# Optimization experiments

Hardware: AMD Instinct MI355X
Metric: run time of the kernel (lower is better)

Reference implementation:

```python
import jax, jax.numpy as jnp
import numpy as np

N_NODES = 100000
N_EDGES = 600000
IN_C, HID_C, OUT_C = 128, 128, 64


def setup_inputs() -> dict:
    key = jax.random.key(0)
    k1, k2, k3, k4 = jax.random.split(key, 4)
    x = jax.random.normal(k1, (N_NODES, IN_C), dtype=jnp.float32)
    edge_index = jax.random.randint(k2, (2, N_EDGES), 0, N_NODES, dtype=jnp.int64)
    # Glorot-ish init for linear weights
    W1 = jax.random.normal(k3, (IN_C, HID_C), dtype=jnp.float32) / np.sqrt(IN_C)
    b1 = jnp.zeros((HID_C,), dtype=jnp.float32)
    W2 = jax.random.normal(k4, (HID_C, OUT_C), dtype=jnp.float32) / np.sqrt(HID_C)
    b2 = jnp.zeros((OUT_C,), dtype=jnp.float32)
    prelu_a = jnp.full((1,), 0.25, dtype=jnp.float32)  # torch nn.PReLU default
    return {"x": x, "edge_index": edge_index, "W1": W1, "b1": b1,
            "W2": W2, "b2": b2, "prelu_a": prelu_a}


def _gcn_conv(x, src, dst, norm, W, b, num_nodes):
    # PyG GCNConv: h = x W; out[i] = sum_{(j->i)} norm_ji * h[j] + b
    h = x @ W                                   # [N, C_out]
    msg = h[src] * norm[:, None]                # [E', C_out] gather + scale
    out = jax.ops.segment_sum(msg, dst, num_segments=num_nodes)
    return out + b


def reference(x, edge_index, W1, b1, W2, b2, prelu_a):
    n = x.shape[0]
    # add self-loops
    loops = jnp.arange(n, dtype=edge_index.dtype)
    src = jnp.concatenate([edge_index[0], loops])
    dst = jnp.concatenate([edge_index[1], loops])
    # symmetric normalization deg^{-1/2}[src] * deg^{-1/2}[dst]
    deg = jax.ops.segment_sum(jnp.ones_like(dst, dtype=x.dtype), dst, num_segments=n)
    dinv = jnp.where(deg > 0, jax.lax.rsqrt(deg), 0.0)
    norm = dinv[src] * dinv[dst]
    # dropout p=0.0 -> identity
    h = _gcn_conv(x, src, dst, norm, W1, b1, n)
    h = jnp.where(h >= 0, h, prelu_a * h)       # PReLU (single shared parameter)
    out = _gcn_conv(h, src, dst, norm, W2, b2, n)
    return out
```

## Files before the change

### kernel.cpp

```cpp
#include <hip/hip_runtime.h>


typedef __attribute__((ext_vector_type(8))) short bf16x8;
typedef __attribute__((ext_vector_type(4))) float f32x4;

#define CAP 96

__device__ inline unsigned short f2bf(float f) {
    unsigned int b = __float_as_uint(f);
    b += 0x7FFFu + ((b >> 16) & 1u);
    return (unsigned short)(b >> 16);
}
__device__ inline float bflo(unsigned int u) { return __uint_as_float(u << 16); }
__device__ inline float bfhi(unsigned int u) { return __uint_as_float(u & 0xFFFF0000u); }

__global__ void k_pre(const float* __restrict__ W1, const float* __restrict__ W2,
                      unsigned short* __restrict__ Wt1, unsigned short* __restrict__ Wt2,
                      int* __restrict__ cnt, int n) {
    int i = blockIdx.x * blockDim.x + threadIdx.x;
    if (i < n) cnt[i] = 0;
    if (i < 128 * 128) {
        int nn = i >> 7, k = i & 127;
        Wt1[i] = f2bf(W1[k * 128 + nn]);
    } else if (i < 128 * 128 + 64 * 128) {
        int j = i - 128 * 128;
        int nn = j >> 7, k = j & 127;
        Wt2[j] = f2bf(W2[k * 64 + nn]);
    }
}

__global__ void k_fill(const int* __restrict__ src, const int* __restrict__ dst,
                       int* __restrict__ cnt, int* __restrict__ bucket, int e) {
    int i = blockIdx.x * blockDim.x + threadIdx.x;
    if (i >= e) return;
    int d = dst[i];
    int pos = atomicAdd(&cnt[d], 1);
    if (pos < CAP) bucket[(size_t)d * CAP + pos] = src[i];
}

template <int BN, bool CVT, bool DINV>
__global__ __launch_bounds__(512) void k_gemm_mfma(
    const void* __restrict__ Asrc, const unsigned short* __restrict__ Wt,
    unsigned short* __restrict__ H, int n,
    const int* __restrict__ cnt, float* __restrict__ dinv) {
    constexpr int PITCH = 136;
    __shared__ unsigned short Bs[BN * PITCH];
    const int tid = threadIdx.x;

    if (DINV) {
        for (int i = blockIdx.x * 512 + tid; i < n; i += gridDim.x * 512)
            dinv[i] = rsqrtf(1.0f + (float)cnt[i]);
    }

    for (int q = tid; q < BN * 16; q += 512) {
        int row = q >> 4, c16 = q & 15;
        *(uint4*)(Bs + row * PITCH + c16 * 8) =
            *(const uint4*)(Wt + row * 128 + c16 * 8);
    }

    const int wave = tid >> 6, lane = tid & 63;
    const int ml = lane & 15;
    const int g = lane >> 4;
    const int stripe = blockIdx.x * 8 + wave;

    int ra = stripe * 16 + ml;
    if (ra >= n) ra = n - 1;

    bf16x8 af[4];
    if (CVT) {
        const float* A = (const float*)Asrc;
#pragma unroll
        for (int ks = 0; ks < 4; ++ks) {
            const float* p = A + (size_t)ra * 128 + ks * 32 + g * 8;
            float4 a0 = *(const float4*)p;
            float4 a1 = *(const float4*)(p + 4);
            uint4 pk;
            pk.x = (unsigned)f2bf(a0.x) | ((unsigned)f2bf(a0.y) << 16);
            pk.y = (unsigned)f2bf(a0.z) | ((unsigned)f2bf(a0.w) << 16);
            pk.z = (unsigned)f2bf(a1.x) | ((unsigned)f2bf(a1.y) << 16);
            pk.w = (unsigned)f2bf(a1.z) | ((unsigned)f2bf(a1.w) << 16);
            af[ks] = *(bf16x8*)&pk;
        }
    } else {
        const unsigned short* A = (const unsigned short*)Asrc;
#pragma unroll
        for (int ks = 0; ks < 4; ++ks)
            af[ks] = *(const bf16x8*)(A + (size_t)ra * 128 + ks * 32 + g * 8);
    }

    __syncthreads();

    constexpr int NCT = BN / 16;
    f32x4 acc[NCT];
#pragma unroll
    for (int ct = 0; ct < NCT; ++ct) acc[ct] = (f32x4){0.f, 0.f, 0.f, 0.f};

#pragma unroll
    for (int ks = 0; ks < 4; ++ks)
#pragma unroll
        for (int ct = 0; ct < NCT; ++ct) {
            bf16x8 b = *(const bf16x8*)(Bs + (size_t)(ct * 16 + ml) * PITCH + ks * 32 + g * 8);
            acc[ct] = __builtin_amdgcn_mfma_f32_16x16x32_bf16(af[ks], b, acc[ct], 0, 0, 0);
        }

#pragma unroll
    for (int ct = 0; ct < NCT; ++ct)
#pragma unroll
        for (int reg = 0; reg < 4; ++reg) {
            int r = stripe * 16 + g * 4 + reg;
            if (r < n) H[(size_t)r * BN + ct * 16 + ml] = f2bf(acc[ct][reg]);
        }
}

template <int COLS, bool PRELU_BF16_OUT>
__global__ void k_gather(const unsigned short* __restrict__ H,
                         const int* __restrict__ cnt, const int* __restrict__ bucket,
                         const float* __restrict__ dinv, const float* __restrict__ b,
                         void* __restrict__ outp, const float* __restrict__ alpha_p,
                         int n) {
    constexpr int NT = COLS / 8;
    constexpr int G = 256 / NT;
    const int tid = threadIdx.x;
    const int node = blockIdx.x * G + tid / NT;
    if (node >= n) return;
    const int c0 = (tid & (NT - 1)) * 8;

    const float di = dinv[node];
    float acc[8];
    {
        uint4 v = *(const uint4*)(H + (size_t)node * COLS + c0);
        float sl = di * di;
        acc[0] = bflo(v.x) * sl + b[c0 + 0];
        acc[1] = bfhi(v.x) * sl + b[c0 + 1];
        acc[2] = bflo(v.y) * sl + b[c0 + 2];
        acc[3] = bfhi(v.y) * sl + b[c0 + 3];
        acc[4] = bflo(v.z) * sl + b[c0 + 4];
        acc[5] = bfhi(v.z) * sl + b[c0 + 5];
        acc[6] = bflo(v.w) * sl + b[c0 + 6];
        acc[7] = bfhi(v.w) * sl + b[c0 + 7];
    }
    int c = cnt[node];
    if (c > CAP) c = CAP;
    const int* bp = bucket + (size_t)node * CAP;
    for (int p = 0; p < c; ++p) {
        int s = bp[p];
        float nrm = dinv[s] * di;
        uint4 v = *(const uint4*)(H + (size_t)s * COLS + c0);
        acc[0] += bflo(v.x) * nrm;
        acc[1] += bfhi(v.x) * nrm;
        acc[2] += bflo(v.y) * nrm;
        acc[3] += bfhi(v.y) * nrm;
        acc[4] += bflo(v.z) * nrm;
        acc[5] += bfhi(v.z) * nrm;
        acc[6] += bflo(v.w) * nrm;
        acc[7] += bfhi(v.w) * nrm;
    }
    if (PRELU_BF16_OUT) {
        float al = alpha_p[0];
        unsigned short o[8];
#pragma unroll
        for (int j = 0; j < 8; ++j) {
            float t = acc[j];
            t = (t >= 0.f) ? t : al * t;
            o[j] = f2bf(t);
        }
        uint4 pk;
        pk.x = (unsigned)o[0] | ((unsigned)o[1] << 16);
        pk.y = (unsigned)o[2] | ((unsigned)o[3] << 16);
        pk.z = (unsigned)o[4] | ((unsigned)o[5] << 16);
        pk.w = (unsigned)o[6] | ((unsigned)o[7] << 16);
        *(uint4*)((unsigned short*)outp + (size_t)node * COLS + c0) = pk;
    } else {
        float* out = (float*)outp;
        *(float4*)(out + (size_t)node * COLS + c0) =
            make_float4(acc[0], acc[1], acc[2], acc[3]);
        *(float4*)(out + (size_t)node * COLS + c0 + 4) =
            make_float4(acc[4], acc[5], acc[6], acc[7]);
    }
}

extern "C" void kernel_launch(void* const* d_in, const int* in_sizes, int n_in,
                              void* d_out, int out_size, void* d_ws, size_t ws_size,
                              hipStream_t stream) {
    const float* x  = (const float*)d_in[0];
    const int*   ei = (const int*)d_in[1];
    const float* W1 = (const float*)d_in[2];
    const float* b1 = (const float*)d_in[3];
    const float* W2 = (const float*)d_in[4];
    const float* b2 = (const float*)d_in[5];
    const float* pa = (const float*)d_in[6];
    float* out = (float*)d_out;

    const int n = in_sizes[0] / 128;
    const int e = in_sizes[1] / 2;
    const int* src = ei;
    const int* dst = ei + e;
    const int B = 256;

    unsigned short* h1  = (unsigned short*)d_ws;
    unsigned short* hp  = h1 + (size_t)n * 128;
    unsigned short* h2  = hp + (size_t)n * 128;
    unsigned short* Wt1 = h2 + (size_t)n * 64;
    unsigned short* Wt2 = Wt1 + 128 * 128;
    float* dinv  = (float*)(Wt2 + 64 * 128);
    int* cnt     = (int*)(dinv + n);
    int* bucket  = cnt + n;

    const int gblk = ((n + 15) / 16 + 7) / 8;

    k_pre<<<(n + B - 1) / B, B, 0, stream>>>(W1, W2, Wt1, Wt2, cnt, n);
    k_fill<<<(e + B - 1) / B, B, 0, stream>>>(src, dst, cnt, bucket, e);
    k_gemm_mfma<128, true, true><<<gblk, 512, 0, stream>>>(x, Wt1, h1, n, cnt, dinv);
    k_gather<128, true><<<(n + 15) / 16, 256, 0, stream>>>(h1, cnt, bucket, dinv,
                                                           b1, hp, pa, n);
    k_gemm_mfma<64, false, false><<<gblk, 512, 0, stream>>>(hp, Wt2, h2, n,
                                                            nullptr, nullptr);
    k_gather<64, false><<<(n + 31) / 32, 256, 0, stream>>>(h2, cnt, bucket, dinv,
                                                           b2, out, nullptr, n);
}
```

Before: 225.3 us.

## Fuse edge bucketing into first GEMM and compute dinv inline in gather

Moves the edge-bucket fill (atomic counting and scatter of source indices) into the tail of the first MFMA GEMM kernel, which removes one launch and lets the scatter overlap with GEMM work. The dinv array is dropped: the gather kernels recompute rsqrt(1+cnt) for the destination and each neighbor. The neighbor loop is unrolled by four, loading indices as int4, to expose more independent memory loads. The trade-off is extra rsqrt work and cnt reads per edge, in both gather passes.

```diff
diff --git a/kernel.cpp b/kernel.cpp
--- a/kernel.cpp
+++ b/kernel.cpp
@@ -29,28 +29,15 @@
     }
 }
 
-__global__ void k_fill(const int* __restrict__ src, const int* __restrict__ dst,
-                       int* __restrict__ cnt, int* __restrict__ bucket, int e) {
-    int i = blockIdx.x * blockDim.x + threadIdx.x;
-    if (i >= e) return;
-    int d = dst[i];
-    int pos = atomicAdd(&cnt[d], 1);
-    if (pos < CAP) bucket[(size_t)d * CAP + pos] = src[i];
-}
-
-template <int BN, bool CVT, bool DINV>
+template <int BN, bool CVT, bool FILL>
 __global__ __launch_bounds__(512) void k_gemm_mfma(
     const void* __restrict__ Asrc, const unsigned short* __restrict__ Wt,
     unsigned short* __restrict__ H, int n,
-    const int* __restrict__ cnt, float* __restrict__ dinv) {
+    const int* __restrict__ esrc, const int* __restrict__ edst,
+    int* __restrict__ cnt, int* __restrict__ bucket, int e) {
     constexpr int PITCH = 136;
     __shared__ unsigned short Bs[BN * PITCH];
     const int tid = threadIdx.x;
-
-    if (DINV) {
-        for (int i = blockIdx.x * 512 + tid; i < n; i += gridDim.x * 512)
-            dinv[i] = rsqrtf(1.0f + (float)cnt[i]);
-    }
 
     for (int q = tid; q < BN * 16; q += 512) {
         int row = q >> 4, c16 = q & 15;
@@ -110,14 +97,21 @@
             int r = stripe * 16 + g * 4 + reg;
             if (r < n) H[(size_t)r * BN + ct * 16 + ml] = f2bf(acc[ct][reg]);
         }
+
+    if (FILL) {
+        for (int i = blockIdx.x * 512 + tid; i < e; i += gridDim.x * 512) {
+            int d = edst[i];
+            int pos = atomicAdd(&cnt[d], 1);
+            if (pos < CAP) bucket[(size_t)d * CAP + pos] = esrc[i];
+        }
+    }
 }
 
 template <int COLS, bool PRELU_BF16_OUT>
 __global__ void k_gather(const unsigned short* __restrict__ H,
                          const int* __restrict__ cnt, const int* __restrict__ bucket,
-                         const float* __restrict__ dinv, const float* __restrict__ b,
-                         void* __restrict__ outp, const float* __restrict__ alpha_p,
-                         int n) {
+                         const float* __restrict__ b, void* __restrict__ outp,
+                         const float* __restrict__ alpha_p, int n) {
     constexpr int NT = COLS / 8;
     constexpr int G = 256 / NT;
     const int tid = threadIdx.x;
@@ -125,7 +119,10 @@
     if (node >= n) return;
     const int c0 = (tid & (NT - 1)) * 8;
 
-    const float di = dinv[node];
+    int c = cnt[node];
+    const float di = rsqrtf(1.0f + (float)c);
+    if (c > CAP) c = CAP;
+
     float acc[8];
     {
         uint4 v = *(const uint4*)(H + (size_t)node * COLS + c0);
@@ -139,22 +136,43 @@
         acc[6] = bflo(v.w) * sl + b[c0 + 6];
         acc[7] = bfhi(v.w) * sl + b[c0 + 7];
     }
-    int c = cnt[node];
-    if (c > CAP) c = CAP;
+
     const int* bp = bucket + (size_t)node * CAP;
-    for (int p = 0; p < c; ++p) {
-        int s = bp[p];
-        float nrm = dinv[s] * di;
-        uint4 v = *(const uint4*)(H + (size_t)s * COLS + c0);
-        acc[0] += bflo(v.x) * nrm;
-        acc[1] += bfhi(v.x) * nrm;
-        acc[2] += bflo(v.y) * nrm;
-        acc[3] += bfhi(v.y) * nrm;
-        acc[4] += bflo(v.z) * nrm;
-        acc[5] += bfhi(v.z) * nrm;
-        acc[6] += bflo(v.w) * nrm;
-        acc[7] += bfhi(v.w) * nrm;
-    }
+    const int nb4 = (c + 3) >> 2;
+    for (int q = 0; q < nb4; ++q) {
+        int4 idx = *(const int4*)(bp + q * 4);
+        int base = q * 4;
+        int s0 = idx.x;
+        int s1 = (base + 1 < c) ? idx.y : s0;
+        int s2 = (base + 2 < c) ? idx.z : s0;
+        int s3 = (base + 3 < c) ? idx.w : s0;
+        int cn0 = cnt[s0], cn1 = cnt[s1], cn2 = cnt[s2], cn3 = cnt[s3];
+        uint4 v0 = *(const uint4*)(H + (size_t)s0 * COLS + c0);
+        uint4 v1 = *(const uint4*)(H + (size_t)s1 * COLS + c0);
+        uint4 v2 = *(const uint4*)(H + (size_t)s2 * COLS + c0);
+        uint4 v3 = *(const uint4*)(H + (size_t)s3 * COLS + c0);
+        float n0 = rsqrtf(1.0f + (float)cn0) * di;
+        float n1 = (base + 1 < c) ? rsqrtf(1.0f + (float)cn1) * di : 0.0f;
+        float n2 = (base + 2 < c) ? rsqrtf(1.0f + (float)cn2) * di : 0.0f;
+        float n3 = (base + 3 < c) ? rsqrtf(1.0f + (float)cn3) * di : 0.0f;
+        acc[0] += bflo(v0.x) * n0; acc[1] += bfhi(v0.x) * n0;
+        acc[2] += bflo(v0.y) * n0; acc[3] += bfhi(v0.y) * n0;
+        acc[4] += bflo(v0.z) * n0; acc[5] += bfhi(v0.z) * n0;
+        acc[6] += bflo(v0.w) * n0; acc[7] += bfhi(v0.w) * n0;
+        acc[0] += bflo(v1.x) * n1; acc[1] += bfhi(v1.x) * n1;
+        acc[2] += bflo(v1.y) * n1; acc[3] += bfhi(v1.y) * n1;
+        acc[4] += bflo(v1.z) * n1; acc[5] += bfhi(v1.z) * n1;
+        acc[6] += bflo(v1.w) * n1; acc[7] += bfhi(v1.w) * n1;
+        acc[0] += bflo(v2.x) * n2; acc[1] += bfhi(v2.x) * n2;
+        acc[2] += bflo(v2.y) * n2; acc[3] += bfhi(v2.y) * n2;
+        acc[4] += bflo(v2.z) * n2; acc[5] += bfhi(v2.z) * n2;
+        acc[6] += bflo(v2.w) * n2; acc[7] += bfhi(v2.w) * n2;
+        acc[0] += bflo(v3.x) * n3; acc[1] += bfhi(v3.x) * n3;
+        acc[2] += bflo(v3.y) * n3; acc[3] += bfhi(v3.y) * n3;
+        acc[4] += bflo(v3.z) * n3; acc[5] += bfhi(v3.z) * n3;
+        acc[6] += bflo(v3.w) * n3; acc[7] += bfhi(v3.w) * n3;
+    }
+
     if (PRELU_BF16_OUT) {
         float al = alpha_p[0];
         unsigned short o[8];
@@ -202,19 +220,18 @@
     unsigned short* h2  = hp + (size_t)n * 128;
     unsigned short* Wt1 = h2 + (size_t)n * 64;
     unsigned short* Wt2 = Wt1 + 128 * 128;
-    float* dinv  = (float*)(Wt2 + 64 * 128);
-    int* cnt     = (int*)(dinv + n);
+    int* cnt     = (int*)(Wt2 + 64 * 128);
     int* bucket  = cnt + n;
 
     const int gblk = ((n + 15) / 16 + 7) / 8;
 
     k_pre<<<(n + B - 1) / B, B, 0, stream>>>(W1, W2, Wt1, Wt2, cnt, n);
-    k_fill<<<(e + B - 1) / B, B, 0, stream>>>(src, dst, cnt, bucket, e);
-    k_gemm_mfma<128, true, true><<<gblk, 512, 0, stream>>>(x, Wt1, h1, n, cnt, dinv);
-    k_gather<128, true><<<(n + 15) / 16, 256, 0, stream>>>(h1, cnt, bucket, dinv,
+    k_gemm_mfma<128, true, true><<<gblk, 512, 0, stream>>>(
+        x, Wt1, h1, n, src, dst, cnt, bucket, e);
+    k_gather<128, true><<<(n + 15) / 16, 256, 0, stream>>>(h1, cnt, bucket,
                                                            b1, hp, pa, n);
-    k_gemm_mfma<64, false, false><<<gblk, 512, 0, stream>>>(hp, Wt2, h2, n,
-                                                            nullptr, nullptr);
-    k_gather<64, false><<<(n + 31) / 32, 256, 0, stream>>>(h2, cnt, bucket, dinv,
+    k_gemm_mfma<64, false, false><<<gblk, 512, 0, stream>>>(
+        hp, Wt2, h2, n, nullptr, nullptr, nullptr, nullptr, 0);
+    k_gather<64, false><<<(n + 31) / 32, 256, 0, stream>>>(h2, cnt, bucket,
                                                            b2, out, nullptr, n);
 }
```

Result: faster. 216.8 us (-3.8%).
